# Performance work log

Measured on AMD Instinct MI355X. Metric: run time of the kernel, lower is better.

## Reference

```python
import jax, jax.numpy as jnp
import numpy as np
import math

HIDDEN = 512
NUM_HEADS = 8
HEAD_DIM = HIDDEN // NUM_HEADS
NUM_BUCKETS = 32
MAX_DISTANCE = 128


def _relative_position_bucket(rel_pos, bidirectional=True):
    # rel_pos: int32 [S, T]
    num_buckets = NUM_BUCKETS
    ret = 0
    if bidirectional:
        num_buckets //= 2
        ret = (rel_pos > 0).astype(jnp.int32) * num_buckets
        rel_pos = jnp.abs(rel_pos)
    else:
        rel_pos = -jnp.minimum(rel_pos, 0)
    max_exact = num_buckets // 2
    is_small = rel_pos < max_exact
    # guard log(0); result unused where is_small
    safe = jnp.maximum(rel_pos, 1).astype(jnp.float32)
    val_if_large = max_exact + (
        jnp.log(safe / max_exact) / math.log(MAX_DISTANCE / max_exact) * (num_buckets - max_exact)
    ).astype(jnp.int32)
    val_if_large = jnp.minimum(val_if_large, num_buckets - 1)
    return ret + jnp.where(is_small, rel_pos, val_if_large)


def setup_inputs() -> dict:
    key = jax.random.key(0)
    ks = jax.random.split(key, 6)
    B, S = 4, 2048
    std = 1.0 / math.sqrt(HIDDEN)
    inp = {
        "x": jax.random.normal(ks[0], (B, S, HIDDEN), dtype=jnp.float32),
        "Wq": jax.random.normal(ks[1], (HIDDEN, HIDDEN), dtype=jnp.float32) * std,
        "Wk": jax.random.normal(ks[2], (HIDDEN, HIDDEN), dtype=jnp.float32) * std,
        "Wv": jax.random.normal(ks[3], (HIDDEN, HIDDEN), dtype=jnp.float32) * std,
        "Wo": jax.random.normal(ks[4], (HIDDEN, HIDDEN), dtype=jnp.float32) * std,
        "bias_table": jax.random.normal(ks[5], (NUM_BUCKETS, NUM_HEADS), dtype=jnp.float32) * 0.02,
    }
    return inp


def reference(x, Wq, Wk, Wv, Wo, bias_table):
    # x: [B, S, HIDDEN]; weights: [HIDDEN, HIDDEN] (out = x @ W.T semantics folded as x @ W here
    # -- weights are random so orientation is a convention; we use x @ W).
    B, S, _ = x.shape
    T = S  # self-attention, context=None
    scale = HEAD_DIM ** -0.5

    def split_heads(t, L):
        return t.reshape(B, L, NUM_HEADS, HEAD_DIM).transpose(0, 2, 1, 3)  # [B,H,L,D]

    q = split_heads(x @ Wq, S)
    k = split_heads(x @ Wk, T)
    v = split_heads(x @ Wv, T)

    # relative position bias: [1, H, S, T]
    rel = jnp.arange(T, dtype=jnp.int32)[None, :] - jnp.arange(S, dtype=jnp.int32)[:, None]
    buckets = _relative_position_bucket(rel, bidirectional=True)  # [S, T]
    pos_bias = bias_table[buckets]  # [S, T, H]
    pos_bias = pos_bias.transpose(2, 0, 1)[None]  # [1, H, S, T]

    attn = jnp.einsum("bhsd,bhtd->bhst", q, k) * scale + pos_bias
    attn = jax.nn.softmax(attn, axis=-1)  # dropout = identity (eval)
    out = jnp.einsum("bhst,bhtd->bhsd", attn, v)
    out = out.transpose(0, 2, 1, 3).reshape(B, S, HIDDEN)
    return out @ Wo
```

## Files before the change

### kernel.cpp

```cpp
#include <hip/hip_runtime.h>
#include <hip/hip_bf16.h>
#include <math.h>

#define HIDDEN 512
#define NHEADS 8
#define HDIM 64
#define SLEN 2048
#define BATCH 4
#define NROWS (BATCH*SLEN)
#define RTAB (2*SLEN-1)
#define LOG2E 1.44269504088896340736f
#define SCALE_L2E (0.125f * LOG2E)

typedef _Float16 f16;
typedef f16 f16x8 __attribute__((ext_vector_type(8)));
typedef float f32x4 __attribute__((ext_vector_type(4)));
typedef unsigned short u16;
typedef unsigned int u32;
typedef u16 u16x4 __attribute__((ext_vector_type(4)));
typedef u16 u16x8 __attribute__((ext_vector_type(8)));
typedef u32 u32x4 __attribute__((ext_vector_type(4)));

__global__ __launch_bounds__(256) void bias_precompute(
    const float* __restrict__ bias_table, float* __restrict__ biasrel) {
  int i = blockIdx.x * 256 + threadIdx.x;
  if (i >= NHEADS * RTAB) return;
  int h = i / RTAB;
  int idx = i - h * RTAB;
  int rel = idx - (SLEN - 1);
  int ret = rel > 0 ? 16 : 0;
  int a = rel < 0 ? -rel : rel;
  int bidx;
  if (a < 8) {
    bidx = a;
  } else {
    float val = logf((float)a * 0.125f) / logf(16.0f) * 8.0f;
    bidx = 8 + (int)val;
    if (bidx > 15) bidx = 15;
  }
  biasrel[i] = bias_table[(ret + bidx) * NHEADS + h] * LOG2E;
}

__global__ __launch_bounds__(256) void conv_x(
    const float* __restrict__ x, u16* __restrict__ xh) {
  int i = blockIdx.x * 256 + threadIdx.x;
  const float4* p = (const float4*)(x + (size_t)i * 8);
  float4 a = p[0], b = p[1];
  u16x8 o;
  f16 t0 = (f16)a.x; o[0] = *(u16*)&t0;
  f16 t1 = (f16)a.y; o[1] = *(u16*)&t1;
  f16 t2 = (f16)a.z; o[2] = *(u16*)&t2;
  f16 t3 = (f16)a.w; o[3] = *(u16*)&t3;
  f16 t4 = (f16)b.x; o[4] = *(u16*)&t4;
  f16 t5 = (f16)b.y; o[5] = *(u16*)&t5;
  f16 t6 = (f16)b.z; o[6] = *(u16*)&t6;
  f16 t7 = (f16)b.w; o[7] = *(u16*)&t7;
  *(u16x8*)(xh + (size_t)i * 8) = o;
}

__global__ __launch_bounds__(256) void conv_w(
    const float* __restrict__ Wq, const float* __restrict__ Wk,
    const float* __restrict__ Wv, const float* __restrict__ Wo,
    u16* __restrict__ Wt) {
  const float* W = blockIdx.y == 0 ? Wq : blockIdx.y == 1 ? Wk
                 : blockIdx.y == 2 ? Wv : Wo;
  u16* dst = Wt + (size_t)blockIdx.y * HIDDEN * HIDDEN;
  int t = blockIdx.x * 256 + threadIdx.x;
  int k = t >> 6, n0 = (t & 63) << 3;
  const float4* p = (const float4*)(W + (size_t)k * HIDDEN + n0);
  float4 a = p[0], b = p[1];
  float vals[8] = {a.x, a.y, a.z, a.w, b.x, b.y, b.z, b.w};
#pragma unroll
  for (int j = 0; j < 8; ++j) {
    f16 hv = (f16)vals[j];
    dst[(size_t)(n0 + j) * HIDDEN + k] = *(u16*)&hv;
  }
}

__global__ __launch_bounds__(256) void gemm_mfma(
    const u16* __restrict__ A, const u16* __restrict__ Wt0,
    const u16* __restrict__ Wt1, const u16* __restrict__ Wt2,
    void* __restrict__ O, int mode) {
  __shared__ u16 sm[2 * 128 * 72];
  u16 (*As)[72] = (u16(*)[72])sm;
  u16 (*Bs)[72] = (u16(*)[72])(sm + 128 * 72);
  const u16* Wt = blockIdx.z == 0 ? Wt0 : blockIdx.z == 1 ? Wt1 : Wt2;
  const int tid = threadIdx.x;
  const int w = tid >> 6, l = tid & 63;
  const int lr = l & 15, lg = l >> 4;
  const int wr = w >> 1, wc = w & 1;
  const int m0 = blockIdx.x << 7, n0 = blockIdx.y << 7;
  const int vtmode = (mode == 1) && (blockIdx.z == 2);

  f32x4 acc[4][4] = {};

  u16x8 areg[4], breg[4];
#pragma unroll
  for (int e = 0; e < 4; ++e) {
    int c = (e << 8) + tid;
    int row = c >> 3, g = c & 7;
    areg[e] = *(const u16x8*)(A + (size_t)(m0 + row) * HIDDEN + (g << 3));
    breg[e] = *(const u16x8*)(Wt + (size_t)(n0 + row) * HIDDEN + (g << 3));
  }

  for (int k0 = 0; k0 < HIDDEN; k0 += 64) {
    __syncthreads();
#pragma unroll
    for (int e = 0; e < 4; ++e) {
      int c = (e << 8) + tid;
      int row = c >> 3, g = c & 7;
      *(u16x8*)&As[row][g << 3] = areg[e];
      *(u16x8*)&Bs[row][g << 3] = breg[e];
    }
    __syncthreads();
    if (k0 + 64 < HIDDEN) {
#pragma unroll
      for (int e = 0; e < 4; ++e) {
        int c = (e << 8) + tid;
        int row = c >> 3, g = c & 7;
        areg[e] = *(const u16x8*)(A + (size_t)(m0 + row) * HIDDEN + k0 + 64 + (g << 3));
        breg[e] = *(const u16x8*)(Wt + (size_t)(n0 + row) * HIDDEN + k0 + 64 + (g << 3));
      }
    }
#pragma unroll
    for (int kk = 0; kk < 64; kk += 32) {
      f16x8 af[4], bf[4];
#pragma unroll
      for (int mt = 0; mt < 4; ++mt)
        af[mt] = *(const f16x8*)&As[(wr << 6) + (mt << 4) + lr][kk + (lg << 3)];
#pragma unroll
      for (int nt = 0; nt < 4; ++nt)
        bf[nt] = *(const f16x8*)&Bs[(wc << 6) + (nt << 4) + lr][kk + (lg << 3)];
      if (!vtmode) {
#pragma unroll
        for (int mt = 0; mt < 4; ++mt)
#pragma unroll
          for (int nt = 0; nt < 4; ++nt)
            acc[mt][nt] = __builtin_amdgcn_mfma_f32_16x16x32_f16(
                af[mt], bf[nt], acc[mt][nt], 0, 0, 0);
      } else {
#pragma unroll
        for (int i = 0; i < 4; ++i)
#pragma unroll
          for (int j = 0; j < 4; ++j)
            acc[i][j] = __builtin_amdgcn_mfma_f32_16x16x32_f16(
                bf[i], af[j], acc[i][j], 0, 0, 0);
      }
    }
  }

  if (mode == 0) {
    float* Of = (float*)O;
#pragma unroll
    for (int mt = 0; mt < 4; ++mt)
#pragma unroll
      for (int nt = 0; nt < 4; ++nt)
#pragma unroll
        for (int r = 0; r < 4; ++r) {
          int m = m0 + (wr << 6) + (mt << 4) + (lg << 2) + r;
          int n = n0 + (wc << 6) + (nt << 4) + lr;
          Of[(size_t)m * HIDDEN + n] = acc[mt][nt][r];
        }
  } else if (!vtmode) {
    __syncthreads();
    u16* tt = sm;
    const float osc = (blockIdx.z == 0) ? SCALE_L2E : 1.0f;
#pragma unroll
    for (int mt = 0; mt < 4; ++mt)
#pragma unroll
      for (int nt = 0; nt < 4; ++nt)
#pragma unroll
        for (int r = 0; r < 4; ++r) {
          int ml = (wr << 6) + (mt << 4) + (lg << 2) + r;
          int nl = (wc << 6) + (nt << 4) + lr;
          f16 hv = (f16)(acc[mt][nt][r] * osc);
          tt[ml * 136 + nl] = *(u16*)&hv;
        }
    __syncthreads();
    u16* O16 = (u16*)O + (size_t)blockIdx.z * NROWS * HIDDEN;
    int b = m0 >> 11, s0 = m0 & (SLEN - 1);
    int hl = tid >> 7, rr = tid & 127;
    int hh = (n0 >> 6) + hl;
    u16* obase = O16 + (((size_t)b * NHEADS + hh) * SLEN + s0) * HDIM;
#pragma unroll
    for (int c = 0; c < 8; ++c) {
      int sl = (rr >> 3) + (c << 4);
      int d8 = (rr & 7) << 3;
      u16x8 v = *(const u16x8*)&tt[sl * 136 + (hl << 6) + d8];
      *(u16x8*)(obase + (size_t)sl * HDIM + d8) = v;
    }
  } else {
    __syncthreads();
    u16* tt = sm;
#pragma unroll
    for (int i = 0; i < 4; ++i)
#pragma unroll
      for (int j = 0; j < 4; ++j)
#pragma unroll
        for (int r = 0; r < 4; ++r) {
          int nl = (wc << 6) + (i << 4) + (lg << 2) + r;
          int ml = (wr << 6) + (j << 4) + lr;
          f16 hv = (f16)acc[i][j][r];
          tt[nl * 136 + ml] = *(u16*)&hv;
        }
    __syncthreads();
    u16* O16 = (u16*)O + (size_t)2 * NROWS * HIDDEN;
    int nl = tid >> 1, half = tid & 1;
    int n = n0 + nl;
    int h = n >> 6, d = n & 63;
    int b = m0 >> 11, s_base = m0 & (SLEN - 1);
    u16* orow = O16 + (((size_t)b * NHEADS + h) * HDIM + d) * SLEN + s_base;
    const u16* trow = tt + nl * 136;
#pragma unroll
    for (int c = 0; c < 8; ++c) {
      int v_off = (half << 6) + (c << 3);
      int c0 = (v_off & ~31) | (((v_off >> 3) & 3) << 2);
      u16x4 lo = *(const u16x4*)(trow + c0);
      u16x4 hi = *(const u16x4*)(trow + c0 + 16);
      u16x8 st;
#pragma unroll
      for (int j = 0; j < 4; ++j) { st[j] = lo[j]; st[j + 4] = hi[j]; }
      *(u16x8*)(orow + v_off) = st;
    }
  }
}

__global__ __launch_bounds__(256) void flash_attn_mfma(
    const u16* __restrict__ qg, const u16* __restrict__ kg,
    const u16* __restrict__ vtg, const float* __restrict__ biasrel,
    u16* __restrict__ attn_out) {
  __shared__ u16 Ks[2][64][72];
  __shared__ u16 Vt[2][64][72];

  const int tid = threadIdx.x;
  const int w = tid >> 6, l = tid & 63;
  const int lr = l & 15, lg = l >> 4;

  int bid = blockIdx.x;
  int xcd = bid & 7, idx = bid >> 3;
  int bh = (xcd << 2) + (idx >> 4);
  int bx = idx & 15;
  int h = bh & 7, b = bh >> 3;
  int q0 = bx << 7;

  const u16* qp = qg + (size_t)bh * (SLEN * HDIM);
  const u16* kp = kg + (size_t)bh * (SLEN * HDIM);
  const u16* vp = vtg + (size_t)bh * (HDIM * SLEN);

  const float bias_pos = biasrel[h * RTAB + 2 * (SLEN - 1)];
  const float bias_neg = biasrel[h * RTAB];

  f16x8 aq[2][2];
#pragma unroll
  for (int sub = 0; sub < 2; ++sub) {
    const u16* qrow = qp + (size_t)(q0 + (w << 5) + (sub << 4) + lr) * HDIM + (lg << 3);
    aq[sub][0] = *(const f16x8*)(qrow);
    aq[sub][1] = *(const f16x8*)(qrow + 32);
  }

  const float* bb = biasrel + h * RTAB + (SLEN - 1) + (lg << 2) - lr - q0 - (w << 5);

  f32x4 acc[2][4] = {};
  f32x4 accl[2] = {};
  const f16x8 ones = {(f16)1.f, (f16)1.f, (f16)1.f, (f16)1.f,
                      (f16)1.f, (f16)1.f, (f16)1.f, (f16)1.f};

  u16x8 kreg[2], vreg[2];
#pragma unroll
  for (int e = 0; e < 2; ++e) {
    int c = tid + (e << 8);
    int row = c >> 3, c8 = (c & 7) << 3;
    kreg[e] = *(const u16x8*)(kp + (size_t)row * HDIM + c8);
    vreg[e] = *(const u16x8*)(vp + (size_t)row * SLEN + c8);
  }
#pragma unroll
  for (int e = 0; e < 2; ++e) {
    int c = tid + (e << 8);
    int row = c >> 3, c8 = (c & 7) << 3;
    *(u16x8*)&Ks[0][row][c8] = kreg[e];
    *(u16x8*)&Vt[0][row][c8] = vreg[e];
  }
#pragma unroll
  for (int e = 0; e < 2; ++e) {
    int c = tid + (e << 8);
    int row = c >> 3, c8 = (c & 7) << 3;
    kreg[e] = *(const u16x8*)(kp + (size_t)(64 + row) * HDIM + c8);
    vreg[e] = *(const u16x8*)(vp + (size_t)row * SLEN + 64 + c8);
  }
  __syncthreads();

  int cur = 0;
  for (int t0 = 0; t0 < SLEN; t0 += 64) {
    if (t0 + 64 < SLEN) {
#pragma unroll
      for (int e = 0; e < 2; ++e) {
        int c = tid + (e << 8);
        int row = c >> 3, c8 = (c & 7) << 3;
        *(u16x8*)&Ks[cur ^ 1][row][c8] = kreg[e];
        *(u16x8*)&Vt[cur ^ 1][row][c8] = vreg[e];
      }
      if (t0 + 128 < SLEN) {
#pragma unroll
        for (int e = 0; e < 2; ++e) {
          int c = tid + (e << 8);
          int row = c >> 3, c8 = (c & 7) << 3;
          kreg[e] = *(const u16x8*)(kp + (size_t)(t0 + 128 + row) * HDIM + c8);
          vreg[e] = *(const u16x8*)(vp + (size_t)row * SLEN + t0 + 128 + c8);
        }
      }
    }

    int dtq = t0 - q0;
    f32x4 sc[2][4];
    if (dtq >= 256 || dtq <= -192) {
      float c = (dtq > 0) ? bias_pos : bias_neg;
      f32x4 cv = {c, c, c, c};
#pragma unroll
      for (int sub = 0; sub < 2; ++sub)
#pragma unroll
        for (int ct = 0; ct < 4; ++ct) sc[sub][ct] = cv;
    } else {
#pragma unroll
      for (int sub = 0; sub < 2; ++sub)
#pragma unroll
        for (int ct = 0; ct < 4; ++ct)
#pragma unroll
          for (int r = 0; r < 4; ++r)
            sc[sub][ct][r] = bb[t0 + (ct << 4) + r - (sub << 4)];
    }

    f16x8 kf[4][2];
#pragma unroll
    for (int ct = 0; ct < 4; ++ct) {
      kf[ct][0] = *(const f16x8*)&Ks[cur][(ct << 4) + lr][lg << 3];
      kf[ct][1] = *(const f16x8*)&Ks[cur][(ct << 4) + lr][32 + (lg << 3)];
    }

    __builtin_amdgcn_s_setprio(1);
#pragma unroll
    for (int sub = 0; sub < 2; ++sub)
#pragma unroll
      for (int ct = 0; ct < 4; ++ct) {
        sc[sub][ct] = __builtin_amdgcn_mfma_f32_16x16x32_f16(
            kf[ct][0], aq[sub][0], sc[sub][ct], 0, 0, 0);
        sc[sub][ct] = __builtin_amdgcn_mfma_f32_16x16x32_f16(
            kf[ct][1], aq[sub][1], sc[sub][ct], 0, 0, 0);
      }
    __builtin_amdgcn_s_setprio(0);

#pragma unroll
    for (int sub = 0; sub < 2; ++sub)
#pragma unroll
      for (int ct = 0; ct < 4; ++ct)
#pragma unroll
        for (int r = 0; r < 4; ++r)
          sc[sub][ct][r] = __builtin_amdgcn_exp2f(sc[sub][ct][r]);

    f16x8 vf[2][4];
#pragma unroll
    for (int kb = 0; kb < 2; ++kb)
#pragma unroll
      for (int dt = 0; dt < 4; ++dt)
        vf[kb][dt] = *(const f16x8*)&Vt[cur][(dt << 4) + lr][(kb << 5) + (lg << 3)];

    __builtin_amdgcn_s_setprio(1);
#pragma unroll
    for (int sub = 0; sub < 2; ++sub)
#pragma unroll
      for (int kb = 0; kb < 2; ++kb) {
        u32 a0 = __builtin_bit_cast(u32,
            __builtin_amdgcn_cvt_pkrtz(sc[sub][2 * kb][0], sc[sub][2 * kb][1]));
        u32 a1 = __builtin_bit_cast(u32,
            __builtin_amdgcn_cvt_pkrtz(sc[sub][2 * kb][2], sc[sub][2 * kb][3]));
        u32 a2 = __builtin_bit_cast(u32,
            __builtin_amdgcn_cvt_pkrtz(sc[sub][2 * kb + 1][0], sc[sub][2 * kb + 1][1]));
        u32 a3 = __builtin_bit_cast(u32,
            __builtin_amdgcn_cvt_pkrtz(sc[sub][2 * kb + 1][2], sc[sub][2 * kb + 1][3]));
        u32x4 pk = {a0, a1, a2, a3};
        f16x8 pa = __builtin_bit_cast(f16x8, pk);
        accl[sub] = __builtin_amdgcn_mfma_f32_16x16x32_f16(
            pa, ones, accl[sub], 0, 0, 0);
#pragma unroll
        for (int dt = 0; dt < 4; ++dt)
          acc[sub][dt] = __builtin_amdgcn_mfma_f32_16x16x32_f16(
              pa, vf[kb][dt], acc[sub][dt], 0, 0, 0);
      }
    __builtin_amdgcn_s_setprio(0);

    __syncthreads();
    cur ^= 1;
  }

#pragma unroll
  for (int sub = 0; sub < 2; ++sub) {
    float linv[4];
#pragma unroll
    for (int r = 0; r < 4; ++r) linv[r] = 1.f / accl[sub][r];
    u16* op = attn_out +
              ((size_t)(b * SLEN) + q0 + (w << 5) + (sub << 4)) * HIDDEN + (h << 6);
#pragma unroll
    for (int r = 0; r < 4; ++r)
#pragma unroll
      for (int dt = 0; dt < 4; ++dt) {
        f16 hv = (f16)(acc[sub][dt][r] * linv[r]);
        op[(size_t)((lg << 2) + r) * HIDDEN + (dt << 4) + lr] = *(u16*)&hv;
      }
  }
}

extern "C" void kernel_launch(void* const* d_in, const int* in_sizes, int n_in,
                              void* d_out, int out_size, void* d_ws, size_t ws_size,
                              hipStream_t stream) {
  const float* x          = (const float*)d_in[0];
  const float* Wq         = (const float*)d_in[1];
  const float* Wk         = (const float*)d_in[2];
  const float* Wv         = (const float*)d_in[3];
  const float* Wo         = (const float*)d_in[4];
  const float* bias_table = (const float*)d_in[5];
  float* out = (float*)d_out;

  u16* xh   = (u16*)d_ws;
  u16* wt   = xh + (size_t)NROWS * HIDDEN;
  u16* qkv  = wt + (size_t)4 * HIDDEN * HIDDEN;
  u16* attno_h = qkv + (size_t)3 * NROWS * HIDDEN;
  float* biasrel = (float*)(attno_h + (size_t)NROWS * HIDDEN);

  u16* qb = qkv;
  u16* kb = qkv + (size_t)NROWS * HIDDEN;
  u16* vb = qkv + (size_t)2 * NROWS * HIDDEN;

  bias_precompute<<<(NHEADS * RTAB + 255) / 256, 256, 0, stream>>>(bias_table, biasrel);
  conv_x<<<NROWS * HIDDEN / 8 / 256, 256, 0, stream>>>(x, xh);
  conv_w<<<dim3(HIDDEN * HIDDEN / 8 / 256, 4), 256, 0, stream>>>(Wq, Wk, Wv, Wo, wt);

  u16* wtq = wt;
  u16* wtk = wt + (size_t)HIDDEN * HIDDEN;
  u16* wtv = wt + (size_t)2 * HIDDEN * HIDDEN;
  u16* wto = wt + (size_t)3 * HIDDEN * HIDDEN;

  gemm_mfma<<<dim3(NROWS / 128, HIDDEN / 128, 3), 256, 0, stream>>>(
      xh, wtq, wtk, wtv, qkv, 1);

  flash_attn_mfma<<<SLEN / 128 * BATCH * NHEADS, 256, 0, stream>>>(
      qb, kb, vb, biasrel, attno_h);

  gemm_mfma<<<dim3(NROWS / 128, HIDDEN / 128, 1), 256, 0, stream>>>(
      attno_h, wto, wto, wto, out, 0);
}
```

Before: 104.8 us.

## Merge prep kernels into one launch and double attention KV tile to 128

Combines the bias-table, x-conversion and weight-conversion kernels into a single prep kernel dispatched by block index, removing two launches. The flash attention loop now stages 128 keys/values per iteration into shared memory instead of 64, processing them as two 64-wide halves, which halves the number of barriers and buffer swaps. This costs more shared memory and more registers for prefetch, which may reduce occupancy.

```diff
diff --git a/kernel.cpp b/kernel.cpp
--- a/kernel.cpp
+++ b/kernel.cpp
@@ -21,59 +21,59 @@
 typedef u16 u16x8 __attribute__((ext_vector_type(8)));
 typedef u32 u32x4 __attribute__((ext_vector_type(4)));
 
-__global__ __launch_bounds__(256) void bias_precompute(
-    const float* __restrict__ bias_table, float* __restrict__ biasrel) {
-  int i = blockIdx.x * 256 + threadIdx.x;
-  if (i >= NHEADS * RTAB) return;
-  int h = i / RTAB;
-  int idx = i - h * RTAB;
-  int rel = idx - (SLEN - 1);
-  int ret = rel > 0 ? 16 : 0;
-  int a = rel < 0 ? -rel : rel;
-  int bidx;
-  if (a < 8) {
-    bidx = a;
+__global__ __launch_bounds__(256) void prep(
+    const float* __restrict__ x, const float* __restrict__ Wq,
+    const float* __restrict__ Wk, const float* __restrict__ Wv,
+    const float* __restrict__ Wo, const float* __restrict__ bias_table,
+    u16* __restrict__ xh, u16* __restrict__ Wt, float* __restrict__ biasrel) {
+  int bid = blockIdx.x;
+  int tid = threadIdx.x;
+  if (bid < 2048) {
+    int i = bid * 256 + tid;
+    const float4* p = (const float4*)(x + (size_t)i * 8);
+    float4 a = p[0], b = p[1];
+    u16x8 o;
+    f16 t0 = (f16)a.x; o[0] = *(u16*)&t0;
+    f16 t1 = (f16)a.y; o[1] = *(u16*)&t1;
+    f16 t2 = (f16)a.z; o[2] = *(u16*)&t2;
+    f16 t3 = (f16)a.w; o[3] = *(u16*)&t3;
+    f16 t4 = (f16)b.x; o[4] = *(u16*)&t4;
+    f16 t5 = (f16)b.y; o[5] = *(u16*)&t5;
+    f16 t6 = (f16)b.z; o[6] = *(u16*)&t6;
+    f16 t7 = (f16)b.w; o[7] = *(u16*)&t7;
+    *(u16x8*)(xh + (size_t)i * 8) = o;
+  } else if (bid < 2560) {
+    int wb = bid - 2048;
+    int wy = wb >> 7;
+    const float* W = wy == 0 ? Wq : wy == 1 ? Wk : wy == 2 ? Wv : Wo;
+    u16* dst = Wt + (size_t)wy * HIDDEN * HIDDEN;
+    int t = (wb & 127) * 256 + tid;
+    int k = t >> 6, n0 = (t & 63) << 3;
+    const float4* p = (const float4*)(W + (size_t)k * HIDDEN + n0);
+    float4 a = p[0], b = p[1];
+    float vals[8] = {a.x, a.y, a.z, a.w, b.x, b.y, b.z, b.w};
+#pragma unroll
+    for (int j = 0; j < 8; ++j) {
+      f16 hv = (f16)vals[j];
+      dst[(size_t)(n0 + j) * HIDDEN + k] = *(u16*)&hv;
+    }
   } else {
-    float val = logf((float)a * 0.125f) / logf(16.0f) * 8.0f;
-    bidx = 8 + (int)val;
-    if (bidx > 15) bidx = 15;
-  }
-  biasrel[i] = bias_table[(ret + bidx) * NHEADS + h] * LOG2E;
-}
-
-__global__ __launch_bounds__(256) void conv_x(
-    const float* __restrict__ x, u16* __restrict__ xh) {
-  int i = blockIdx.x * 256 + threadIdx.x;
-  const float4* p = (const float4*)(x + (size_t)i * 8);
-  float4 a = p[0], b = p[1];
-  u16x8 o;
-  f16 t0 = (f16)a.x; o[0] = *(u16*)&t0;
-  f16 t1 = (f16)a.y; o[1] = *(u16*)&t1;
-  f16 t2 = (f16)a.z; o[2] = *(u16*)&t2;
-  f16 t3 = (f16)a.w; o[3] = *(u16*)&t3;
-  f16 t4 = (f16)b.x; o[4] = *(u16*)&t4;
-  f16 t5 = (f16)b.y; o[5] = *(u16*)&t5;
-  f16 t6 = (f16)b.z; o[6] = *(u16*)&t6;
-  f16 t7 = (f16)b.w; o[7] = *(u16*)&t7;
-  *(u16x8*)(xh + (size_t)i * 8) = o;
-}
-
-__global__ __launch_bounds__(256) void conv_w(
-    const float* __restrict__ Wq, const float* __restrict__ Wk,
-    const float* __restrict__ Wv, const float* __restrict__ Wo,
-    u16* __restrict__ Wt) {
-  const float* W = blockIdx.y == 0 ? Wq : blockIdx.y == 1 ? Wk
-                 : blockIdx.y == 2 ? Wv : Wo;
-  u16* dst = Wt + (size_t)blockIdx.y * HIDDEN * HIDDEN;
-  int t = blockIdx.x * 256 + threadIdx.x;
-  int k = t >> 6, n0 = (t & 63) << 3;
-  const float4* p = (const float4*)(W + (size_t)k * HIDDEN + n0);
-  float4 a = p[0], b = p[1];
-  float vals[8] = {a.x, a.y, a.z, a.w, b.x, b.y, b.z, b.w};
-#pragma unroll
-  for (int j = 0; j < 8; ++j) {
-    f16 hv = (f16)vals[j];
-    dst[(size_t)(n0 + j) * HIDDEN + k] = *(u16*)&hv;
+    int i = (bid - 2560) * 256 + tid;
+    if (i >= NHEADS * RTAB) return;
+    int h = i / RTAB;
+    int idx = i - h * RTAB;
+    int rel = idx - (SLEN - 1);
+    int ret = rel > 0 ? 16 : 0;
+    int a = rel < 0 ? -rel : rel;
+    int bidx;
+    if (a < 8) {
+      bidx = a;
+    } else {
+      float val = logf((float)a * 0.125f) / logf(16.0f) * 8.0f;
+      bidx = 8 + (int)val;
+      if (bidx > 15) bidx = 15;
+    }
+    biasrel[i] = bias_table[(ret + bidx) * NHEADS + h] * LOG2E;
   }
 }
 
@@ -229,8 +229,8 @@
     const u16* __restrict__ qg, const u16* __restrict__ kg,
     const u16* __restrict__ vtg, const float* __restrict__ biasrel,
     u16* __restrict__ attn_out) {
-  __shared__ u16 Ks[2][64][72];
-  __shared__ u16 Vt[2][64][72];
+  __shared__ u16 Ks[2][128][72];
+  __shared__ u16 Vt[2][64][136];
 
   const int tid = threadIdx.x;
   const int w = tid >> 6, l = tid & 63;
@@ -265,127 +265,136 @@
   const f16x8 ones = {(f16)1.f, (f16)1.f, (f16)1.f, (f16)1.f,
                       (f16)1.f, (f16)1.f, (f16)1.f, (f16)1.f};
 
-  u16x8 kreg[2], vreg[2];
-#pragma unroll
-  for (int e = 0; e < 2; ++e) {
+  u16x8 kreg[4], vreg[4];
+#pragma unroll
+  for (int e = 0; e < 4; ++e) {
     int c = tid + (e << 8);
-    int row = c >> 3, c8 = (c & 7) << 3;
-    kreg[e] = *(const u16x8*)(kp + (size_t)row * HDIM + c8);
-    vreg[e] = *(const u16x8*)(vp + (size_t)row * SLEN + c8);
-  }
-#pragma unroll
-  for (int e = 0; e < 2; ++e) {
+    int krow = c >> 3, kc8 = (c & 7) << 3;
+    kreg[e] = *(const u16x8*)(kp + (size_t)krow * HDIM + kc8);
+    int vrow = c >> 4, vc8 = (c & 15) << 3;
+    vreg[e] = *(const u16x8*)(vp + (size_t)vrow * SLEN + vc8);
+  }
+#pragma unroll
+  for (int e = 0; e < 4; ++e) {
     int c = tid + (e << 8);
-    int row = c >> 3, c8 = (c & 7) << 3;
-    *(u16x8*)&Ks[0][row][c8] = kreg[e];
-    *(u16x8*)&Vt[0][row][c8] = vreg[e];
-  }
-#pragma unroll
-  for (int e = 0; e < 2; ++e) {
+    int krow = c >> 3, kc8 = (c & 7) << 3;
+    *(u16x8*)&Ks[0][krow][kc8] = kreg[e];
+    int vrow = c >> 4, vc8 = (c & 15) << 3;
+    *(u16x8*)&Vt[0][vrow][vc8] = vreg[e];
+  }
+#pragma unroll
+  for (int e = 0; e < 4; ++e) {
     int c = tid + (e << 8);
-    int row = c >> 3, c8 = (c & 7) << 3;
-    kreg[e] = *(const u16x8*)(kp + (size_t)(64 + row) * HDIM + c8);
-    vreg[e] = *(const u16x8*)(vp + (size_t)row * SLEN + 64 + c8);
+    int krow = c >> 3, kc8 = (c & 7) << 3;
+    kreg[e] = *(const u16x8*)(kp + (size_t)(128 + krow) * HDIM + kc8);
+    int vrow = c >> 4, vc8 = (c & 15) << 3;
+    vreg[e] = *(const u16x8*)(vp + (size_t)vrow * SLEN + 128 + vc8);
   }
   __syncthreads();
 
   int cur = 0;
-  for (int t0 = 0; t0 < SLEN; t0 += 64) {
-    if (t0 + 64 < SLEN) {
-#pragma unroll
-      for (int e = 0; e < 2; ++e) {
+  for (int t0 = 0; t0 < SLEN; t0 += 128) {
+    if (t0 + 128 < SLEN) {
+#pragma unroll
+      for (int e = 0; e < 4; ++e) {
         int c = tid + (e << 8);
-        int row = c >> 3, c8 = (c & 7) << 3;
-        *(u16x8*)&Ks[cur ^ 1][row][c8] = kreg[e];
-        *(u16x8*)&Vt[cur ^ 1][row][c8] = vreg[e];
-      }
-      if (t0 + 128 < SLEN) {
-#pragma unroll
-        for (int e = 0; e < 2; ++e) {
+        int krow = c >> 3, kc8 = (c & 7) << 3;
+        *(u16x8*)&Ks[cur ^ 1][krow][kc8] = kreg[e];
+        int vrow = c >> 4, vc8 = (c & 15) << 3;
+        *(u16x8*)&Vt[cur ^ 1][vrow][vc8] = vreg[e];
+      }
+      if (t0 + 256 < SLEN) {
+#pragma unroll
+        for (int e = 0; e < 4; ++e) {
           int c = tid + (e << 8);
-          int row = c >> 3, c8 = (c & 7) << 3;
-          kreg[e] = *(const u16x8*)(kp + (size_t)(t0 + 128 + row) * HDIM + c8);
-          vreg[e] = *(const u16x8*)(vp + (size_t)row * SLEN + t0 + 128 + c8);
-        }
-      }
-    }
-
-    int dtq = t0 - q0;
-    f32x4 sc[2][4];
-    if (dtq >= 256 || dtq <= -192) {
-      float c = (dtq > 0) ? bias_pos : bias_neg;
-      f32x4 cv = {c, c, c, c};
+          int krow = c >> 3, kc8 = (c & 7) << 3;
+          kreg[e] = *(const u16x8*)(kp + (size_t)(t0 + 256 + krow) * HDIM + kc8);
+          int vrow = c >> 4, vc8 = (c & 15) << 3;
+          vreg[e] = *(const u16x8*)(vp + (size_t)vrow * SLEN + t0 + 256 + vc8);
+        }
+      }
+    }
+
+#pragma unroll
+    for (int hf = 0; hf < 2; ++hf) {
+      const int kvb = hf << 6;
+      int dtq = t0 + kvb - q0;
+      f32x4 sc[2][4];
+      if (dtq >= 256 || dtq <= -192) {
+        float c = (dtq > 0) ? bias_pos : bias_neg;
+        f32x4 cv = {c, c, c, c};
+#pragma unroll
+        for (int sub = 0; sub < 2; ++sub)
+#pragma unroll
+          for (int ct = 0; ct < 4; ++ct) sc[sub][ct] = cv;
+      } else {
+#pragma unroll
+        for (int sub = 0; sub < 2; ++sub)
+#pragma unroll
+          for (int ct = 0; ct < 4; ++ct)
+#pragma unroll
+            for (int r = 0; r < 4; ++r)
+              sc[sub][ct][r] = bb[t0 + kvb + (ct << 4) + r - (sub << 4)];
+      }
+
+      f16x8 kf[4][2];
+#pragma unroll
+      for (int ct = 0; ct < 4; ++ct) {
+        kf[ct][0] = *(const f16x8*)&Ks[cur][kvb + (ct << 4) + lr][lg << 3];
+        kf[ct][1] = *(const f16x8*)&Ks[cur][kvb + (ct << 4) + lr][32 + (lg << 3)];
+      }
+
+      __builtin_amdgcn_s_setprio(1);
 #pragma unroll
       for (int sub = 0; sub < 2; ++sub)
 #pragma unroll
-        for (int ct = 0; ct < 4; ++ct) sc[sub][ct] = cv;
-    } else {
+        for (int ct = 0; ct < 4; ++ct) {
+          sc[sub][ct] = __builtin_amdgcn_mfma_f32_16x16x32_f16(
+              kf[ct][0], aq[sub][0], sc[sub][ct], 0, 0, 0);
+          sc[sub][ct] = __builtin_amdgcn_mfma_f32_16x16x32_f16(
+              kf[ct][1], aq[sub][1], sc[sub][ct], 0, 0, 0);
+        }
+      __builtin_amdgcn_s_setprio(0);
+
 #pragma unroll
       for (int sub = 0; sub < 2; ++sub)
 #pragma unroll
         for (int ct = 0; ct < 4; ++ct)
 #pragma unroll
           for (int r = 0; r < 4; ++r)
-            sc[sub][ct][r] = bb[t0 + (ct << 4) + r - (sub << 4)];
-    }
-
-    f16x8 kf[4][2];
-#pragma unroll
-    for (int ct = 0; ct < 4; ++ct) {
-      kf[ct][0] = *(const f16x8*)&Ks[cur][(ct << 4) + lr][lg << 3];
-      kf[ct][1] = *(const f16x8*)&Ks[cur][(ct << 4) + lr][32 + (lg << 3)];
-    }
-
-    __builtin_amdgcn_s_setprio(1);
-#pragma unroll
-    for (int sub = 0; sub < 2; ++sub)
-#pragma unroll
-      for (int ct = 0; ct < 4; ++ct) {
-        sc[sub][ct] = __builtin_amdgcn_mfma_f32_16x16x32_f16(
-            kf[ct][0], aq[sub][0], sc[sub][ct], 0, 0, 0);
-        sc[sub][ct] = __builtin_amdgcn_mfma_f32_16x16x32_f16(
-            kf[ct][1], aq[sub][1], sc[sub][ct], 0, 0, 0);
-      }
-    __builtin_amdgcn_s_setprio(0);
-
-#pragma unroll
-    for (int sub = 0; sub < 2; ++sub)
-#pragma unroll
-      for (int ct = 0; ct < 4; ++ct)
-#pragma unroll
-        for (int r = 0; r < 4; ++r)
-          sc[sub][ct][r] = __builtin_amdgcn_exp2f(sc[sub][ct][r]);
-
-    f16x8 vf[2][4];
-#pragma unroll
-    for (int kb = 0; kb < 2; ++kb)
-#pragma unroll
-      for (int dt = 0; dt < 4; ++dt)
-        vf[kb][dt] = *(const f16x8*)&Vt[cur][(dt << 4) + lr][(kb << 5) + (lg << 3)];
-
-    __builtin_amdgcn_s_setprio(1);
-#pragma unroll
-    for (int sub = 0; sub < 2; ++sub)
-#pragma unroll
-      for (int kb = 0; kb < 2; ++kb) {
-        u32 a0 = __builtin_bit_cast(u32,
-            __builtin_amdgcn_cvt_pkrtz(sc[sub][2 * kb][0], sc[sub][2 * kb][1]));
-        u32 a1 = __builtin_bit_cast(u32,
-            __builtin_amdgcn_cvt_pkrtz(sc[sub][2 * kb][2], sc[sub][2 * kb][3]));
-        u32 a2 = __builtin_bit_cast(u32,
-            __builtin_amdgcn_cvt_pkrtz(sc[sub][2 * kb + 1][0], sc[sub][2 * kb + 1][1]));
-        u32 a3 = __builtin_bit_cast(u32,
-            __builtin_amdgcn_cvt_pkrtz(sc[sub][2 * kb + 1][2], sc[sub][2 * kb + 1][3]));
-        u32x4 pk = {a0, a1, a2, a3};
-        f16x8 pa = __builtin_bit_cast(f16x8, pk);
-        accl[sub] = __builtin_amdgcn_mfma_f32_16x16x32_f16(
-            pa, ones, accl[sub], 0, 0, 0);
+            sc[sub][ct][r] = __builtin_amdgcn_exp2f(sc[sub][ct][r]);
+
+      f16x8 vf[2][4];
+#pragma unroll
+      for (int kb = 0; kb < 2; ++kb)
 #pragma unroll
         for (int dt = 0; dt < 4; ++dt)
-          acc[sub][dt] = __builtin_amdgcn_mfma_f32_16x16x32_f16(
-              pa, vf[kb][dt], acc[sub][dt], 0, 0, 0);
-      }
-    __builtin_amdgcn_s_setprio(0);
+          vf[kb][dt] = *(const f16x8*)&Vt[cur][(dt << 4) + lr][kvb + (kb << 5) + (lg << 3)];
+
+      __builtin_amdgcn_s_setprio(1);
+#pragma unroll
+      for (int sub = 0; sub < 2; ++sub)
+#pragma unroll
+        for (int kb = 0; kb < 2; ++kb) {
+          u32 a0 = __builtin_bit_cast(u32,
+              __builtin_amdgcn_cvt_pkrtz(sc[sub][2 * kb][0], sc[sub][2 * kb][1]));
+          u32 a1 = __builtin_bit_cast(u32,
+              __builtin_amdgcn_cvt_pkrtz(sc[sub][2 * kb][2], sc[sub][2 * kb][3]));
+          u32 a2 = __builtin_bit_cast(u32,
+              __builtin_amdgcn_cvt_pkrtz(sc[sub][2 * kb + 1][0], sc[sub][2 * kb + 1][1]));
+          u32 a3 = __builtin_bit_cast(u32,
+              __builtin_amdgcn_cvt_pkrtz(sc[sub][2 * kb + 1][2], sc[sub][2 * kb + 1][3]));
+          u32x4 pk = {a0, a1, a2, a3};
+          f16x8 pa = __builtin_bit_cast(f16x8, pk);
+          accl[sub] = __builtin_amdgcn_mfma_f32_16x16x32_f16(
+              pa, ones, accl[sub], 0, 0, 0);
+#pragma unroll
+          for (int dt = 0; dt < 4; ++dt)
+            acc[sub][dt] = __builtin_amdgcn_mfma_f32_16x16x32_f16(
+                pa, vf[kb][dt], acc[sub][dt], 0, 0, 0);
+        }
+      __builtin_amdgcn_s_setprio(0);
+    }
 
     __syncthreads();
     cur ^= 1;
@@ -429,9 +438,7 @@
   u16* kb = qkv + (size_t)NROWS * HIDDEN;
   u16* vb = qkv + (size_t)2 * NROWS * HIDDEN;
 
-  bias_precompute<<<(NHEADS * RTAB + 255) / 256, 256, 0, stream>>>(bias_table, biasrel);
-  conv_x<<<NROWS * HIDDEN / 8 / 256, 256, 0, stream>>>(x, xh);
-  conv_w<<<dim3(HIDDEN * HIDDEN / 8 / 256, 4), 256, 0, stream>>>(Wq, Wk, Wv, Wo, wt);
+  prep<<<2688, 256, 0, stream>>>(x, Wq, Wk, Wv, Wo, bias_table, xh, wt, biasrel);
 
   u16* wtq = wt;
   u16* wtk = wt + (size_t)HIDDEN * HIDDEN;
```

Result: faster. 100.6 us (median of 2 runs) (-4.0%).

## Halve attention query tile to 64 rows and merge prep kernels into one launch

Applied to the files above, without the earlier changes.

The flash attention kernel now gives each block 64 query rows instead of 128, so each wave handles 16 rows and the grid doubles to 1024 blocks, with launch bounds asking for 4 blocks per CU. This is meant to raise occupancy and fill the CUs better, but every K/V tile is now loaded from global memory twice as often, and the ratio of MFMA work to LDS traffic per tile is lower. Separately, the bias-table, x-conversion and weight-conversion kernels are merged into a single prep launch to cut launch overhead.

```diff
diff --git a/kernel.cpp b/kernel.cpp
--- a/kernel.cpp
+++ b/kernel.cpp
@@ -21,59 +21,59 @@
 typedef u16 u16x8 __attribute__((ext_vector_type(8)));
 typedef u32 u32x4 __attribute__((ext_vector_type(4)));
 
-__global__ __launch_bounds__(256) void bias_precompute(
-    const float* __restrict__ bias_table, float* __restrict__ biasrel) {
-  int i = blockIdx.x * 256 + threadIdx.x;
-  if (i >= NHEADS * RTAB) return;
-  int h = i / RTAB;
-  int idx = i - h * RTAB;
-  int rel = idx - (SLEN - 1);
-  int ret = rel > 0 ? 16 : 0;
-  int a = rel < 0 ? -rel : rel;
-  int bidx;
-  if (a < 8) {
-    bidx = a;
+__global__ __launch_bounds__(256) void prep(
+    const float* __restrict__ x, const float* __restrict__ Wq,
+    const float* __restrict__ Wk, const float* __restrict__ Wv,
+    const float* __restrict__ Wo, const float* __restrict__ bias_table,
+    u16* __restrict__ xh, u16* __restrict__ Wt, float* __restrict__ biasrel) {
+  int bid = blockIdx.x;
+  int tid = threadIdx.x;
+  if (bid < 2048) {
+    int i = bid * 256 + tid;
+    const float4* p = (const float4*)(x + (size_t)i * 8);
+    float4 a = p[0], b = p[1];
+    u16x8 o;
+    f16 t0 = (f16)a.x; o[0] = *(u16*)&t0;
+    f16 t1 = (f16)a.y; o[1] = *(u16*)&t1;
+    f16 t2 = (f16)a.z; o[2] = *(u16*)&t2;
+    f16 t3 = (f16)a.w; o[3] = *(u16*)&t3;
+    f16 t4 = (f16)b.x; o[4] = *(u16*)&t4;
+    f16 t5 = (f16)b.y; o[5] = *(u16*)&t5;
+    f16 t6 = (f16)b.z; o[6] = *(u16*)&t6;
+    f16 t7 = (f16)b.w; o[7] = *(u16*)&t7;
+    *(u16x8*)(xh + (size_t)i * 8) = o;
+  } else if (bid < 2560) {
+    int wb = bid - 2048;
+    int wy = wb >> 7;
+    const float* W = wy == 0 ? Wq : wy == 1 ? Wk : wy == 2 ? Wv : Wo;
+    u16* dst = Wt + (size_t)wy * HIDDEN * HIDDEN;
+    int t = (wb & 127) * 256 + tid;
+    int k = t >> 6, n0 = (t & 63) << 3;
+    const float4* p = (const float4*)(W + (size_t)k * HIDDEN + n0);
+    float4 a = p[0], b = p[1];
+    float vals[8] = {a.x, a.y, a.z, a.w, b.x, b.y, b.z, b.w};
+#pragma unroll
+    for (int j = 0; j < 8; ++j) {
+      f16 hv = (f16)vals[j];
+      dst[(size_t)(n0 + j) * HIDDEN + k] = *(u16*)&hv;
+    }
   } else {
-    float val = logf((float)a * 0.125f) / logf(16.0f) * 8.0f;
-    bidx = 8 + (int)val;
-    if (bidx > 15) bidx = 15;
-  }
-  biasrel[i] = bias_table[(ret + bidx) * NHEADS + h] * LOG2E;
-}
-
-__global__ __launch_bounds__(256) void conv_x(
-    const float* __restrict__ x, u16* __restrict__ xh) {
-  int i = blockIdx.x * 256 + threadIdx.x;
-  const float4* p = (const float4*)(x + (size_t)i * 8);
-  float4 a = p[0], b = p[1];
-  u16x8 o;
-  f16 t0 = (f16)a.x; o[0] = *(u16*)&t0;
-  f16 t1 = (f16)a.y; o[1] = *(u16*)&t1;
-  f16 t2 = (f16)a.z; o[2] = *(u16*)&t2;
-  f16 t3 = (f16)a.w; o[3] = *(u16*)&t3;
-  f16 t4 = (f16)b.x; o[4] = *(u16*)&t4;
-  f16 t5 = (f16)b.y; o[5] = *(u16*)&t5;
-  f16 t6 = (f16)b.z; o[6] = *(u16*)&t6;
-  f16 t7 = (f16)b.w; o[7] = *(u16*)&t7;
-  *(u16x8*)(xh + (size_t)i * 8) = o;
-}
-
-__global__ __launch_bounds__(256) void conv_w(
-    const float* __restrict__ Wq, const float* __restrict__ Wk,
-    const float* __restrict__ Wv, const float* __restrict__ Wo,
-    u16* __restrict__ Wt) {
-  const float* W = blockIdx.y == 0 ? Wq : blockIdx.y == 1 ? Wk
-                 : blockIdx.y == 2 ? Wv : Wo;
-  u16* dst = Wt + (size_t)blockIdx.y * HIDDEN * HIDDEN;
-  int t = blockIdx.x * 256 + threadIdx.x;
-  int k = t >> 6, n0 = (t & 63) << 3;
-  const float4* p = (const float4*)(W + (size_t)k * HIDDEN + n0);
-  float4 a = p[0], b = p[1];
-  float vals[8] = {a.x, a.y, a.z, a.w, b.x, b.y, b.z, b.w};
-#pragma unroll
-  for (int j = 0; j < 8; ++j) {
-    f16 hv = (f16)vals[j];
-    dst[(size_t)(n0 + j) * HIDDEN + k] = *(u16*)&hv;
+    int i = (bid - 2560) * 256 + tid;
+    if (i >= NHEADS * RTAB) return;
+    int h = i / RTAB;
+    int idx = i - h * RTAB;
+    int rel = idx - (SLEN - 1);
+    int ret = rel > 0 ? 16 : 0;
+    int a = rel < 0 ? -rel : rel;
+    int bidx;
+    if (a < 8) {
+      bidx = a;
+    } else {
+      float val = logf((float)a * 0.125f) / logf(16.0f) * 8.0f;
+      bidx = 8 + (int)val;
+      if (bidx > 15) bidx = 15;
+    }
+    biasrel[i] = bias_table[(ret + bidx) * NHEADS + h] * LOG2E;
   }
 }
 
@@ -225,7 +225,7 @@
   }
 }
 
-__global__ __launch_bounds__(256) void flash_attn_mfma(
+__global__ __launch_bounds__(256, 4) void flash_attn_mfma(
     const u16* __restrict__ qg, const u16* __restrict__ kg,
     const u16* __restrict__ vtg, const float* __restrict__ biasrel,
     u16* __restrict__ attn_out) {
@@ -238,10 +238,10 @@
 
   int bid = blockIdx.x;
   int xcd = bid & 7, idx = bid >> 3;
-  int bh = (xcd << 2) + (idx >> 4);
-  int bx = idx & 15;
+  int bh = (xcd << 2) + (idx >> 5);
+  int bx = idx & 31;
   int h = bh & 7, b = bh >> 3;
-  int q0 = bx << 7;
+  int q0 = bx << 6;
 
   const u16* qp = qg + (size_t)bh * (SLEN * HDIM);
   const u16* kp = kg + (size_t)bh * (SLEN * HDIM);
@@ -250,18 +250,17 @@
   const float bias_pos = biasrel[h * RTAB + 2 * (SLEN - 1)];
   const float bias_neg = biasrel[h * RTAB];
 
-  f16x8 aq[2][2];
-#pragma unroll
-  for (int sub = 0; sub < 2; ++sub) {
-    const u16* qrow = qp + (size_t)(q0 + (w << 5) + (sub << 4) + lr) * HDIM + (lg << 3);
-    aq[sub][0] = *(const f16x8*)(qrow);
-    aq[sub][1] = *(const f16x8*)(qrow + 32);
-  }
-
-  const float* bb = biasrel + h * RTAB + (SLEN - 1) + (lg << 2) - lr - q0 - (w << 5);
-
-  f32x4 acc[2][4] = {};
-  f32x4 accl[2] = {};
+  f16x8 aq0, aq1;
+  {
+    const u16* qrow = qp + (size_t)(q0 + (w << 4) + lr) * HDIM + (lg << 3);
+    aq0 = *(const f16x8*)(qrow);
+    aq1 = *(const f16x8*)(qrow + 32);
+  }
+
+  const float* bb = biasrel + h * RTAB + (SLEN - 1) + (lg << 2) - lr - q0 - (w << 4);
+
+  f32x4 acc[4] = {};
+  f32x4 accl = {};
   const f16x8 ones = {(f16)1.f, (f16)1.f, (f16)1.f, (f16)1.f,
                       (f16)1.f, (f16)1.f, (f16)1.f, (f16)1.f};
 
@@ -311,22 +310,18 @@
     }
 
     int dtq = t0 - q0;
-    f32x4 sc[2][4];
-    if (dtq >= 256 || dtq <= -192) {
+    f32x4 sc[4];
+    if (dtq >= 192 || dtq <= -192) {
       float c = (dtq > 0) ? bias_pos : bias_neg;
       f32x4 cv = {c, c, c, c};
 #pragma unroll
-      for (int sub = 0; sub < 2; ++sub)
-#pragma unroll
-        for (int ct = 0; ct < 4; ++ct) sc[sub][ct] = cv;
+      for (int ct = 0; ct < 4; ++ct) sc[ct] = cv;
     } else {
 #pragma unroll
-      for (int sub = 0; sub < 2; ++sub)
-#pragma unroll
-        for (int ct = 0; ct < 4; ++ct)
-#pragma unroll
-          for (int r = 0; r < 4; ++r)
-            sc[sub][ct][r] = bb[t0 + (ct << 4) + r - (sub << 4)];
+      for (int ct = 0; ct < 4; ++ct)
+#pragma unroll
+        for (int r = 0; r < 4; ++r)
+          sc[ct][r] = bb[t0 + (ct << 4) + r];
     }
 
     f16x8 kf[4][2];
@@ -338,23 +333,19 @@
 
     __builtin_amdgcn_s_setprio(1);
 #pragma unroll
-    for (int sub = 0; sub < 2; ++sub)
-#pragma unroll
-      for (int ct = 0; ct < 4; ++ct) {
-        sc[sub][ct] = __builtin_amdgcn_mfma_f32_16x16x32_f16(
-            kf[ct][0], aq[sub][0], sc[sub][ct], 0, 0, 0);
-        sc[sub][ct] = __builtin_amdgcn_mfma_f32_16x16x32_f16(
-            kf[ct][1], aq[sub][1], sc[sub][ct], 0, 0, 0);
-      }
+    for (int ct = 0; ct < 4; ++ct) {
+      sc[ct] = __builtin_amdgcn_mfma_f32_16x16x32_f16(
+          kf[ct][0], aq0, sc[ct], 0, 0, 0);
+      sc[ct] = __builtin_amdgcn_mfma_f32_16x16x32_f16(
+          kf[ct][1], aq1, sc[ct], 0, 0, 0);
+    }
     __builtin_amdgcn_s_setprio(0);
 
 #pragma unroll
-    for (int sub = 0; sub < 2; ++sub)
-#pragma unroll
-      for (int ct = 0; ct < 4; ++ct)
-#pragma unroll
-        for (int r = 0; r < 4; ++r)
-          sc[sub][ct][r] = __builtin_amdgcn_exp2f(sc[sub][ct][r]);
+    for (int ct = 0; ct < 4; ++ct)
+#pragma unroll
+      for (int r = 0; r < 4; ++r)
+        sc[ct][r] = __builtin_amdgcn_exp2f(sc[ct][r]);
 
     f16x8 vf[2][4];
 #pragma unroll
@@ -365,44 +356,40 @@
 
     __builtin_amdgcn_s_setprio(1);
 #pragma unroll
-    for (int sub = 0; sub < 2; ++sub)
-#pragma unroll
-      for (int kb = 0; kb < 2; ++kb) {
-        u32 a0 = __builtin_bit_cast(u32,
-            __builtin_amdgcn_cvt_pkrtz(sc[sub][2 * kb][0], sc[sub][2 * kb][1]));
-        u32 a1 = __builtin_bit_cast(u32,
-            __builtin_amdgcn_cvt_pkrtz(sc[sub][2 * kb][2], sc[sub][2 * kb][3]));
-        u32 a2 = __builtin_bit_cast(u32,
-            __builtin_amdgcn_cvt_pkrtz(sc[sub][2 * kb + 1][0], sc[sub][2 * kb + 1][1]));
-        u32 a3 = __builtin_bit_cast(u32,
-            __builtin_amdgcn_cvt_pkrtz(sc[sub][2 * kb + 1][2], sc[sub][2 * kb + 1][3]));
-        u32x4 pk = {a0, a1, a2, a3};
-        f16x8 pa = __builtin_bit_cast(f16x8, pk);
-        accl[sub] = __builtin_amdgcn_mfma_f32_16x16x32_f16(
-            pa, ones, accl[sub], 0, 0, 0);
-#pragma unroll
-        for (int dt = 0; dt < 4; ++dt)
-          acc[sub][dt] = __builtin_amdgcn_mfma_f32_16x16x32_f16(
-              pa, vf[kb][dt], acc[sub][dt], 0, 0, 0);
-      }
+    for (int kb = 0; kb < 2; ++kb) {
+      u32 a0 = __builtin_bit_cast(u32,
+          __builtin_amdgcn_cvt_pkrtz(sc[2 * kb][0], sc[2 * kb][1]));
+      u32 a1 = __builtin_bit_cast(u32,
+          __builtin_amdgcn_cvt_pkrtz(sc[2 * kb][2], sc[2 * kb][3]));
+      u32 a2 = __builtin_bit_cast(u32,
+          __builtin_amdgcn_cvt_pkrtz(sc[2 * kb + 1][0], sc[2 * kb + 1][1]));
+      u32 a3 = __builtin_bit_cast(u32,
+          __builtin_amdgcn_cvt_pkrtz(sc[2 * kb + 1][2], sc[2 * kb + 1][3]));
+      u32x4 pk = {a0, a1, a2, a3};
+      f16x8 pa = __builtin_bit_cast(f16x8, pk);
+      accl = __builtin_amdgcn_mfma_f32_16x16x32_f16(pa, ones, accl, 0, 0, 0);
+#pragma unroll
+      for (int dt = 0; dt < 4; ++dt)
+        acc[dt] = __builtin_amdgcn_mfma_f32_16x16x32_f16(
+            pa, vf[kb][dt], acc[dt], 0, 0, 0);
+    }
     __builtin_amdgcn_s_setprio(0);
 
     __syncthreads();
     cur ^= 1;
   }
 
-#pragma unroll
-  for (int sub = 0; sub < 2; ++sub) {
+  {
     float linv[4];
 #pragma unroll
-    for (int r = 0; r < 4; ++r) linv[r] = 1.f / accl[sub][r];
+    for (int r = 0; r < 4; ++r) linv[r] = 1.f / accl[r];
     u16* op = attn_out +
-              ((size_t)(b * SLEN) + q0 + (w << 5) + (sub << 4)) * HIDDEN + (h << 6);
+              ((size_t)(b * SLEN) + q0 + (w << 4)) * HIDDEN + (h << 6);
 #pragma unroll
     for (int r = 0; r < 4; ++r)
 #pragma unroll
       for (int dt = 0; dt < 4; ++dt) {
-        f16 hv = (f16)(acc[sub][dt][r] * linv[r]);
+        f16 hv = (f16)(acc[dt][r] * linv[r]);
         op[(size_t)((lg << 2) + r) * HIDDEN + (dt << 4) + lr] = *(u16*)&hv;
       }
   }
@@ -429,9 +416,7 @@
   u16* kb = qkv + (size_t)NROWS * HIDDEN;
   u16* vb = qkv + (size_t)2 * NROWS * HIDDEN;
 
-  bias_precompute<<<(NHEADS * RTAB + 255) / 256, 256, 0, stream>>>(bias_table, biasrel);
-  conv_x<<<NROWS * HIDDEN / 8 / 256, 256, 0, stream>>>(x, xh);
-  conv_w<<<dim3(HIDDEN * HIDDEN / 8 / 256, 4), 256, 0, stream>>>(Wq, Wk, Wv, Wo, wt);
+  prep<<<2688, 256, 0, stream>>>(x, Wq, Wk, Wv, Wo, bias_table, xh, wt, biasrel);
 
   u16* wtq = wt;
   u16* wtk = wt + (size_t)HIDDEN * HIDDEN;
@@ -441,7 +426,7 @@
   gemm_mfma<<<dim3(NROWS / 128, HIDDEN / 128, 3), 256, 0, stream>>>(
       xh, wtq, wtk, wtv, qkv, 1);
 
-  flash_attn_mfma<<<SLEN / 128 * BATCH * NHEADS, 256, 0, stream>>>(
+  flash_attn_mfma<<<SLEN / 64 * BATCH * NHEADS, 256, 0, stream>>>(
       qb, kb, vb, biasrel, attno_h);
 
   gemm_mfma<<<dim3(NROWS / 128, HIDDEN / 128, 1), 256, 0, stream>>>(
```

Result: slower. 108.9 us (+3.9%).
